# Kernel optimization log

Hardware: AMD Instinct MI355X
Metric: run time of the kernel (lower is better)

## Reference

```python
import jax, jax.numpy as jnp
import numpy as np
from jax.scipy.special import logsumexp

WORD_DIM = 512
SCRF_DIM = 256
N_TAGS = 12
ALLOWED_SPAN = 8
START_ID = 10
STOP_ID = 11
SEQ_LEN = 768
N_SPANS = 96


def _compute_scores(h, Wl, bl, Wr, br, Gl, bgl, Gr, bgr, Wt, bt, transitions):
    # h: [1, L, D] already projected by Dense
    Lc, D = h.shape[1], h.shape[2]
    scores = jnp.zeros((1, Lc, Lc, D), h.dtype)
    diag = jnp.arange(Lc)
    ht = h
    scores = scores.at[:, diag, diag].set(ht)
    for sl in range(1, min(ALLOWED_SPAN, Lc)):
        l, r = ht[:, :-1], ht[:, 1:]
        h_hat = 4.0 * jax.nn.sigmoid(l @ Wl.T + bl + r @ Wr.T + br) - 2.0
        # exp/normalize over 3 gates == softmax over gate axis
        g = (l @ Gl.T + bgl + r @ Gr.T + bgr).reshape(1, Lc - sl, 3, D)
        wgt = jax.nn.softmax(g, axis=2)
        ht = wgt[:, :, 0] * h_hat + wgt[:, :, 1] * l + wgt[:, :, 2] * r
        scores = scores.at[:, diag[:Lc - sl], diag[sl:]].set(ht)
    tagsc = scores @ Wt.T + bt  # [1, L, L, T]
    # final[b,i,j,prev,tag] = tagsc[b,i,j,tag] + transitions[prev,tag]
    return tagsc[:, :, :, None, :] + transitions[None, None, None]


def _forward_pass(s5):
    # s5: [1, L, L, T, T]; semi-Markov forward algorithm, windows of width <= ALLOWED_SPAN
    Lc, T = s5.shape[1], s5.shape[3]
    A = ALLOWED_SPAN
    i0 = jnp.arange(1, Lc + 1)
    k = jnp.arange(A)
    p = i0[:, None] - A + k[None, :]              # candidate span-start positions [L, A]
    m = p >= 0                                    # valid window mask (istarts = max(0, i-A))
    x = s5[0][jnp.clip(p, 0), (i0 - 1)[:, None]]  # [L, A, T, T] span scores ending at i-1
    buf0 = jnp.full((A, T), -10000.0, s5.dtype).at[A - 1, START_ID].set(0.0)

    def step(buf, inp):
        xi, mi = inp
        # tmp[k, prev, tag] = score + logalpha[start, prev]
        tmp = jnp.where(mi[:, None, None], xi + buf[:, :, None], -1e30)
        na = logsumexp(tmp, axis=(0, 1))  # [T]
        return jnp.concatenate([buf[1:], na[None]], axis=0), na

    _, alphas = jax.lax.scan(step, buf0, (x, m))
    return alphas[-1, :STOP_ID].sum()


def _gold_score(s5, tags):
    Lc, T = s5.shape[1], s5.shape[3]
    gf = tags[:, :, 0] * (Lc * T * T) + tags[:, :, 1] * (T * T) + tags[:, :, 2] * T + tags[:, :, 3]
    return jnp.take_along_axis(s5.reshape(1, -1), gf, axis=1).sum()


def setup_inputs() -> dict:
    key = jax.random.key(0)
    ks = jax.random.split(key, 16)
    D, W3 = SCRF_DIM, 3 * SCRF_DIM
    s = 0.05
    def w(k, shape):
        return jax.random.normal(k, shape, dtype=jnp.float32) * s
    return {
        "feats": jax.random.normal(ks[0], (1, SEQ_LEN, WORD_DIM), dtype=jnp.float32),
        "tags": jax.random.randint(ks[1], (1, N_SPANS, 4), 0, N_TAGS),
        "Wd": w(ks[2], (D, WORD_DIM)), "bd": jnp.zeros((D,), jnp.float32),
        "Wl": w(ks[3], (D, D)), "bl": jnp.zeros((D,), jnp.float32),
        "Wr": w(ks[4], (D, D)), "br": jnp.zeros((D,), jnp.float32),
        "Gl": w(ks[5], (W3, D)), "bgl": jnp.zeros((W3,), jnp.float32),
        "Gr": w(ks[6], (W3, D)), "bgr": jnp.zeros((W3,), jnp.float32),
        "Wt": w(ks[7], (N_TAGS, D)), "bt": jnp.zeros((N_TAGS,), jnp.float32),
        "transitions": w(ks[8], (N_TAGS, N_TAGS)),
    }


def reference(feats, tags, Wd, bd, Wl, bl, Wr, br, Gl, bgl, Gr, bgr, Wt, bt, transitions):
    h = feats @ Wd.T + bd  # Dense: word_dim -> scrf_dim
    s5 = _compute_scores(h, Wl, bl, Wr, br, Gl, bgl, Gr, bgr, Wt, bt, transitions)
    gold = _gold_score(s5, tags)
    logZ = _forward_pass(s5)
    return logZ - gold
```

## Files before the change

### kernel.cpp

```cpp
#include <hip/hip_runtime.h>

typedef __attribute__((ext_vector_type(8))) short short8;
typedef __attribute__((ext_vector_type(4))) float f32x4;

__device__ __forceinline__ float bf2f(short s) {
  return __uint_as_float(((unsigned)(unsigned short)s) << 16);
}
__device__ __forceinline__ unsigned short f2bf(float f) {
  unsigned u = __float_as_uint(f);
  unsigned rounding = 0x7fffu + ((u >> 16) & 1u);
  return (unsigned short)((u + rounding) >> 16);
}

__global__ void prep_kernel(const float* __restrict__ feats, const float* __restrict__ Wd,
                            const float* __restrict__ Wl, const float* __restrict__ Wr,
                            const float* __restrict__ Gl, const float* __restrict__ Gr,
                            const float* __restrict__ bl, const float* __restrict__ br,
                            const float* __restrict__ bgl, const float* __restrict__ bgr,
                            unsigned short* __restrict__ featsB, unsigned short* __restrict__ WdB,
                            unsigned short* __restrict__ WcB, float* __restrict__ bc)
{
  int idx = blockIdx.x * 256 + threadIdx.x;
  if (idx < 393216) {
    featsB[idx] = f2bf(feats[idx]);
  } else if (idx < 524288) {
    int j = idx - 393216;
    WdB[j] = f2bf(Wd[j]);
  } else if (idx < 1048576) {
    int j = idx - 524288;
    int o = j >> 9, k = j & 511;
    float v;
    if (k < 256) v = (o < 256) ? Wl[o*256 + k] : Gl[(o-256)*256 + k];
    else { int k2 = k - 256; v = (o < 256) ? Wr[o*256 + k2] : Gr[(o-256)*256 + k2]; }
    WcB[j] = f2bf(v);
  } else if (idx < 1049600) {
    int o = idx - 1048576;
    bc[o] = (o < 256) ? bl[o] + br[o] : bgl[o-256] + bgr[o-256];
  }
}

__global__ __launch_bounds__(256) void hgemm_kernel(const unsigned short* __restrict__ A,
                                                    const unsigned short* __restrict__ W,
                                                    const float* __restrict__ bd,
                                                    unsigned short* __restrict__ C)
{
  __shared__ __align__(16) unsigned short As[64][72];
  __shared__ __align__(16) unsigned short Ws[64][72];
  int p0 = blockIdx.x * 64;
  int n0 = blockIdx.y * 64;
  int tid = threadIdx.x;
  int wave = tid >> 6, lane = tid & 63;
  f32x4 acc[4];
  #pragma unroll
  for (int i = 0; i < 4; ++i)
    #pragma unroll
    for (int j = 0; j < 4; ++j) acc[i][j] = 0.f;

  int lr = tid >> 3;
  int c8 = (tid & 7) * 8;
  for (int kt = 0; kt < 8; ++kt) {
    int kb = kt * 64;
    #pragma unroll
    for (int rr = 0; rr < 64; rr += 32) {
      int row = lr + rr;
      *(short8*)(&As[row][c8]) = *(const short8*)(A + (size_t)(p0 + row)*512 + kb + c8);
      *(short8*)(&Ws[row][c8]) = *(const short8*)(W + (size_t)(n0 + row)*512 + kb + c8);
    }
    __syncthreads();
    int q8 = (lane >> 4) * 8;
    #pragma unroll
    for (int kk = 0; kk < 2; ++kk) {
      short8 b = *(const short8*)(&Ws[wave*16 + (lane & 15)][kk*32 + q8]);
      #pragma unroll
      for (int mt = 0; mt < 4; ++mt) {
        short8 a = *(const short8*)(&As[mt*16 + (lane & 15)][kk*32 + q8]);
        acc[mt] = __builtin_amdgcn_mfma_f32_16x16x32_bf16(a, b, acc[mt], 0, 0, 0);
      }
    }
    __syncthreads();
  }
  int o = n0 + wave*16 + (lane & 15);
  float bias = bd[o];
  #pragma unroll
  for (int mt = 0; mt < 4; ++mt)
    #pragma unroll
    for (int r = 0; r < 4; ++r) {
      int row = p0 + mt*16 + (lane >> 4)*4 + r;
      C[row*256 + o] = f2bf(acc[mt][r] + bias);
    }
}

__global__ __launch_bounds__(256) void iter_kernel(const unsigned short* __restrict__ htp,
                                                   const unsigned short* __restrict__ Wc,
                                                   const float* __restrict__ bc,
                                                   unsigned short* __restrict__ htn,
                                                   int Mvalid)
{
  __shared__ __align__(16) unsigned short As[64][72];
  __shared__ __align__(16) unsigned short Ws[64][72];
  __shared__ float Cs[64][64];
  int p0 = blockIdx.x * 64;
  int n0 = blockIdx.y * 16;
  int tid = threadIdx.x;
  int wave = tid >> 6, lane = tid & 63;
  f32x4 acc[4];
  #pragma unroll
  for (int i = 0; i < 4; ++i)
    #pragma unroll
    for (int j = 0; j < 4; ++j) acc[i][j] = 0.f;

  int lr = tid >> 3;
  int c8 = (tid & 7) * 8;
  for (int kt = 0; kt < 8; ++kt) {
    int kb = kt * 64;
    int shift = kb >> 8;
    int kcol = kb & 255;
    #pragma unroll
    for (int rr = 0; rr < 64; rr += 32) {
      int row = lr + rr;
      int grow = p0 + row + shift; if (grow > 767) grow = 767;
      *(short8*)(&As[row][c8]) = *(const short8*)(htp + (size_t)grow*256 + kcol + c8);
      int o = (row >> 4)*256 + n0 + (row & 15);
      *(short8*)(&Ws[row][c8]) = *(const short8*)(Wc + (size_t)o*512 + kb + c8);
    }
    __syncthreads();
    int q8 = (lane >> 4) * 8;
    #pragma unroll
    for (int kk = 0; kk < 2; ++kk) {
      short8 b = *(const short8*)(&Ws[wave*16 + (lane & 15)][kk*32 + q8]);
      #pragma unroll
      for (int mt = 0; mt < 4; ++mt) {
        short8 a = *(const short8*)(&As[mt*16 + (lane & 15)][kk*32 + q8]);
        acc[mt] = __builtin_amdgcn_mfma_f32_16x16x32_bf16(a, b, acc[mt], 0, 0, 0);
      }
    }
    __syncthreads();
  }
  #pragma unroll
  for (int mt = 0; mt < 4; ++mt)
    #pragma unroll
    for (int r = 0; r < 4; ++r)
      Cs[mt*16 + (lane >> 4)*4 + r][wave*16 + (lane & 15)] = acc[mt][r];
  __syncthreads();

  int dl = tid & 15;
  int d = n0 + dl;
  float bz = bc[d], b0 = bc[256 + d], b1 = bc[512 + d], b2v = bc[768 + d];
  for (int pr = tid >> 4; pr < 64; pr += 16) {
    int p = p0 + pr;
    if (p >= Mvalid) continue;
    float z  = Cs[pr][dl]      + bz;
    float g0 = Cs[pr][16 + dl] + b0;
    float g1 = Cs[pr][32 + dl] + b1;
    float g2 = Cs[pr][48 + dl] + b2v;
    float l = bf2f((short)htp[p*256 + d]);
    float r = bf2f((short)htp[(p+1)*256 + d]);
    float hh = 4.f / (1.f + __expf(-z)) - 2.f;
    float mg = fmaxf(g0, fmaxf(g1, g2));
    float e0 = __expf(g0 - mg), e1 = __expf(g1 - mg), e2 = __expf(g2 - mg);
    float inv = 1.f / (e0 + e1 + e2);
    htn[p*256 + d] = f2bf((e0*hh + e1*l + e2*r) * inv);
  }
}

__global__ __launch_bounds__(128) void band_kernel(const unsigned short* __restrict__ htall,
                                                   const float* __restrict__ Wt,
                                                   const float* __restrict__ bt,
                                                   float* __restrict__ Bband,
                                                   float* __restrict__ Xn,
                                                   float* __restrict__ mu)
{
  __shared__ __align__(16) unsigned short rows[8][264];
  __shared__ float sred[96];
  __shared__ float smu;
  int i = blockIdx.x + 1;
  int tid = threadIdx.x;
  for (int q = tid; q < 256; q += 128) {
    int k = q >> 5, cc = (q & 31) * 8;
    int p = i - 8 + k, sl = 7 - k;
    short8 v;
    if (p >= 0) {
      v = *(const short8*)(htall + ((size_t)sl*768 + p)*256 + cc);
    } else {
      for (int j = 0; j < 8; ++j) v[j] = 0;
    }
    *(short8*)(&rows[k][cc]) = v;
  }
  __syncthreads();
  float res = -1e30f;
  if (tid < 96) {
    int t = tid >> 3, k = tid & 7;
    int p = i - 8 + k;
    if (p >= 0) {
      float acc = 0.f;
      for (int dch = 0; dch < 256; dch += 8) {
        float4 wa = *(const float4*)(Wt + t*256 + dch);
        float4 wb = *(const float4*)(Wt + t*256 + dch + 4);
        short8 hv = *(const short8*)(&rows[k][dch]);
        acc += wa.x*bf2f(hv[0]) + wa.y*bf2f(hv[1]) + wa.z*bf2f(hv[2]) + wa.w*bf2f(hv[3])
             + wb.x*bf2f(hv[4]) + wb.y*bf2f(hv[5]) + wb.z*bf2f(hv[6]) + wb.w*bf2f(hv[7]);
      }
      res = acc + bt[t];
    }
    Bband[(size_t)i*96 + tid] = res;
    sred[tid] = res;
  }
  __syncthreads();
  if (tid < 32) {
    float m = fmaxf(sred[tid], fmaxf(sred[tid+32], sred[tid+64]));
    #pragma unroll
    for (int off = 16; off; off >>= 1) m = fmaxf(m, __shfl_down(m, off));
    if (tid == 0) { mu[i] = m; smu = m; }
  }
  __syncthreads();
  if (tid < 96) Xn[(size_t)i*96 + tid] = __expf(res - smu);
}

__global__ __launch_bounds__(256) void chunkT_kernel(const float* __restrict__ Xn,
                                                     const float* __restrict__ mu,
                                                     const float* __restrict__ trans,
                                                     float* __restrict__ T,
                                                     float* __restrict__ C0)
{
  int chunk = blockIdx.y;
  int a = chunk * 16;
  int tid = threadIdx.x;
  if (blockIdx.x == 0 && tid == 0) C0[chunk] = 0.f;
  int wv = tid >> 6;
  int lane = tid & 63;
  int g = lane / 12;
  int t = lane - g * 12;
  int cidx = blockIdx.x * 20 + wv * 5 + g;
  bool active = (g < 5) && (cidx < 96);
  int c = active ? cidx : 95;
  int s = c / 12, tau = c - s * 12;
  float Etc[12];
  #pragma unroll
  for (int j = 0; j < 12; ++j) Etc[j] = __expf(trans[j*12 + t]);
  float NA[8], V[8];
  #pragma unroll
  for (int j = 0; j < 8; ++j) { NA[j] = 0.f; V[j] = 0.f; }
  #pragma unroll
  for (int j = 0; j < 8; ++j) if (j == s) {
    NA[j] = (t == tau) ? 1.f : 0.f;
    V[j]  = Etc[tau];
  }
  int gb = (g * 12) * 4;
  #pragma unroll
  for (int m = 1; m <= 16; ++m) {
    const float* xr = Xn + (size_t)(a + m) * 96 + t * 8;
    float4 x0 = *(const float4*)xr;
    float4 x1 = *(const float4*)(xr + 4);
    float sf = __expf(-mu[a + m]);
    float na = x0.x*V[0] + x0.y*V[1] + x0.z*V[2] + x0.w*V[3]
             + x1.x*V[4] + x1.y*V[5] + x1.z*V[6] + x1.w*V[7];
    int nai = __float_as_int(na);
    float nb[12];
    #pragma unroll
    for (int j = 0; j < 12; ++j)
      nb[j] = __int_as_float(__builtin_amdgcn_ds_bpermute(gb + j*4, nai));
    float p0 = nb[0]*Etc[0] + nb[1]*Etc[1] + nb[2]*Etc[2]  + nb[3]*Etc[3];
    float p1 = nb[4]*Etc[4] + nb[5]*Etc[5] + nb[6]*Etc[6]  + nb[7]*Etc[7];
    float p2 = nb[8]*Etc[8] + nb[9]*Etc[9] + nb[10]*Etc[10] + nb[11]*Etc[11];
    float v = (p0 + p1) + p2;
    #pragma unroll
    for (int k = 0; k < 7; ++k) { NA[k] = NA[k+1]*sf; V[k] = V[k+1]*sf; }
    NA[7] = na; V[7] = v;
  }
  if (active) {
    float* dst = T + (size_t)chunk * 9216 + c;
    #pragma unroll
    for (int j = 0; j < 8; ++j) dst[(size_t)(j*12 + t) * 96] = NA[j];
  }
}

#define TPAD 100
__global__ __launch_bounds__(256) void treemul_kernel(const float* __restrict__ Tin,
                                                      const float* __restrict__ Cin,
                                                      float* __restrict__ Tout,
                                                      float* __restrict__ Cout)
{
  __shared__ float Bs[96 * TPAD];
  __shared__ float Acs[96 * TPAD];
  __shared__ float red[8];
  int j = blockIdx.y;
  int cs = blockIdx.x * 48;
  const float* Ag = Tin + (size_t)(2*j) * 9216;
  const float* Bg = Tin + (size_t)(2*j + 1) * 9216;
  int tid = threadIdx.x;
  int wv = tid >> 6, lane = tid & 63;

  float4 av[9], bv[9];
  const float* ap = Ag + tid * 36;
  const float* bp = Bg + tid * 36;
  #pragma unroll
  for (int q = 0; q < 9; ++q) av[q] = *(const float4*)(ap + q*4);
  #pragma unroll
  for (int q = 0; q < 9; ++q) bv[q] = *(const float4*)(bp + q*4);
  float ma = 0.f, mb = 0.f;
  #pragma unroll
  for (int q = 0; q < 9; ++q) {
    ma = fmaxf(ma, fmaxf(fmaxf(av[q].x, av[q].y), fmaxf(av[q].z, av[q].w)));
    mb = fmaxf(mb, fmaxf(fmaxf(bv[q].x, bv[q].y), fmaxf(bv[q].z, bv[q].w)));
  }
  #pragma unroll
  for (int off = 32; off; off >>= 1) {
    ma = fmaxf(ma, __shfl_down(ma, off));
    mb = fmaxf(mb, __shfl_down(mb, off));
  }
  if (lane == 0) { red[wv] = ma; red[4 + wv] = mb; }
  __syncthreads();
  float fa = fmaxf(fmaxf(red[0], red[1]), fmaxf(red[2], red[3]));
  float fb = fmaxf(fmaxf(red[4], red[5]), fmaxf(red[6], red[7]));
  float ia = 1.0f / fa, ib = 1.0f / fb;

  #pragma unroll
  for (int q = 0; q < 9; ++q) {
    int e = tid*36 + q*4;
    int r = e / 96, k = e - r*96;
    float4 b = bv[q];
    b.x *= ib; b.y *= ib; b.z *= ib; b.w *= ib;
    *(float4*)&Bs[r*TPAD + k] = b;
    float4 a = av[q];
    Acs[(k+0)*TPAD + r] = a.x * ia;
    Acs[(k+1)*TPAD + r] = a.y * ia;
    Acs[(k+2)*TPAD + r] = a.z * ia;
    Acs[(k+3)*TPAD + r] = a.w * ia;
  }
  __syncthreads();

  int tr = tid >> 4, tc = tid & 15;
  int r0 = tr * 6, c0 = cs + tc * 3;
  float acc[6][3];
  #pragma unroll
  for (int i = 0; i < 6; ++i)
    #pragma unroll
    for (int m = 0; m < 3; ++m) acc[i][m] = 0.f;
  for (int k = 0; k < 96; k += 4) {
    float4 a0 = *(const float4*)&Acs[(c0+0)*TPAD + k];
    float4 a1 = *(const float4*)&Acs[(c0+1)*TPAD + k];
    float4 a2 = *(const float4*)&Acs[(c0+2)*TPAD + k];
    #pragma unroll
    for (int i = 0; i < 6; ++i) {
      float4 b = *(const float4*)&Bs[(r0+i)*TPAD + k];
      acc[i][0] += b.x*a0.x + b.y*a0.y + b.z*a0.z + b.w*a0.w;
      acc[i][1] += b.x*a1.x + b.y*a1.y + b.z*a1.z + b.w*a1.w;
      acc[i][2] += b.x*a2.x + b.y*a2.y + b.z*a2.z + b.w*a2.w;
    }
  }
  float* op = Tout + (size_t)j * 9216;
  #pragma unroll
  for (int i = 0; i < 6; ++i)
    #pragma unroll
    for (int m = 0; m < 3; ++m)
      op[(size_t)(r0+i)*96 + c0 + m] = acc[i][m];
  if (blockIdx.x == 0 && tid == 0)
    Cout[j] = Cin[2*j] + Cin[2*j + 1] + __logf(fa) + __logf(fb);
}

__global__ __launch_bounds__(256, 1) void final_kernel(const float* __restrict__ Tm,
    const float* __restrict__ Cm, const float* __restrict__ Bband,
    const float* __restrict__ mu, const float* __restrict__ trans,
    const float* __restrict__ bt, const int* __restrict__ tags,
    float* __restrict__ out)
{
  __shared__ float Qs[2][96 * TPAD];
  __shared__ float vv[4][96];
  __shared__ float red[8];
  __shared__ float redm[4];
  int tid = threadIdx.x;
  int wv = tid >> 6, lane = tid & 63;

  float4 P[9];
  const float* p0 = Tm + tid * 36;
  #pragma unroll
  for (int q = 0; q < 9; ++q) P[q] = *(const float4*)(p0 + q*4);

  float gold = 0.f;
  if (tid < 96) {
    int a = tags[tid*4+0], b = tags[tid*4+1], cc = tags[tid*4+2], d = tags[tid*4+3];
    float v = trans[cc*12 + d];
    int sl = b - a;
    if (sl >= 0 && sl < 8) v += Bband[(size_t)(b+1)*96 + d*8 + (7 - sl)];
    else v += bt[d];
    gold = v;
  }
  float mp = 0.f;
  for (int q = tid; q < 768; q += 256) mp += mu[1 + q];
  #pragma unroll
  for (int off = 32; off; off >>= 1) {
    gold += __shfl_down(gold, off);
    mp   += __shfl_down(mp, off);
  }
  if (lane == 0) { red[wv] = gold; red[4 + wv] = mp; }

  #pragma unroll
  for (int q = 0; q < 9; ++q) {
    int e = tid*36 + q*4;
    int r = e / 96, k = e - r*96;
    *(float4*)&Qs[0][r*TPAD + k] = P[q];
  }
  if (tid < 96) vv[0][tid] = (tid == 94) ? 1.f : 0.f;
  __syncthreads();
  float gold_t = red[0] + red[1] + red[2] + red[3];
  float musum  = red[4] + red[5] + red[6] + red[7];
  float Ct = Cm[0] + Cm[1] + Cm[2];

  #pragma unroll
  for (int s = 0; s < 3; ++s) {
    if (s < 2) {
      const float* pn = Tm + (size_t)(s+1)*9216 + tid*36;
      #pragma unroll
      for (int q = 0; q < 9; ++q) P[q] = *(const float4*)(pn + q*4);
    }
    float acc = 0.f;
    if (tid < 96) {
      const float* Qr = &Qs[s & 1][tid * TPAD];
      #pragma unroll
      for (int k = 0; k < 96; k += 4) {
        float4 qv = *(const float4*)(Qr + k);
        float4 zv = *(const float4*)&vv[s][k];
        acc += qv.x*zv.x + qv.y*zv.y + qv.z*zv.z + qv.w*zv.w;
      }
    }
    float am = (tid < 96) ? acc : 0.f;
    #pragma unroll
    for (int off = 32; off; off >>= 1) am = fmaxf(am, __shfl_down(am, off));
    if (lane == 0) redm[wv] = am;
    __syncthreads();
    float mx = fmaxf(fmaxf(redm[0], redm[1]), fmaxf(redm[2], redm[3]));
    Ct += __logf(mx);
    if (tid < 96) vv[s+1][tid] = acc / mx;
    if (s < 2) {
      #pragma unroll
      for (int q = 0; q < 9; ++q) {
        int e = tid*36 + q*4;
        int r = e / 96, k = e - r*96;
        *(float4*)&Qs[(s+1)&1][r*TPAD + k] = P[q];
      }
    }
    __syncthreads();
  }
  if (tid == 0) {
    float lsum = 0.f;
    #pragma unroll
    for (int t = 0; t < 11; ++t) lsum += __logf(vv[3][84 + t]);
    out[0] = lsum + 11.f * (Ct + musum) - gold_t;
  }
}

extern "C" void kernel_launch(void* const* d_in, const int* in_sizes, int n_in,
                              void* d_out, int out_size, void* d_ws, size_t ws_size,
                              hipStream_t stream)
{
  const float* feats = (const float*)d_in[0];
  const int*   tags  = (const int*)  d_in[1];
  const float* Wd    = (const float*)d_in[2];
  const float* bd    = (const float*)d_in[3];
  const float* Wl    = (const float*)d_in[4];
  const float* bl    = (const float*)d_in[5];
  const float* Wr    = (const float*)d_in[6];
  const float* br    = (const float*)d_in[7];
  const float* Gl    = (const float*)d_in[8];
  const float* bgl   = (const float*)d_in[9];
  const float* Gr    = (const float*)d_in[10];
  const float* bgr   = (const float*)d_in[11];
  const float* Wt    = (const float*)d_in[12];
  const float* bt    = (const float*)d_in[13];
  const float* trans = (const float*)d_in[14];
  float* out = (float*)d_out;

  char* ws = (char*)d_ws;
  unsigned short* featsB = (unsigned short*)(ws + 0);
  unsigned short* WdB    = (unsigned short*)(ws + 786432);
  unsigned short* WcB    = (unsigned short*)(ws + 1048576);
  float*          bc     = (float*)         (ws + 2097152);
  unsigned short* ht     = (unsigned short*)(ws + 2101248);
  float*          Bband  = (float*)         (ws + 5246976);
  float*          Xn     = (float*)         (ws + 5542272);
  float*          muv    = (float*)         (ws + 5837568);
  float*          T      = (float*)         (ws + 5841664);
  float*          Tb     = (float*)         (ws + 0);
  float*          C0     = (float*)         (ws + 1048576);
  float*          Ca     = (float*)         (ws + 1048832);
  float*          Cb     = (float*)         (ws + 1049088);

  prep_kernel<<<4100, 256, 0, stream>>>(feats, Wd, Wl, Wr, Gl, Gr, bl, br, bgl, bgr,
                                        featsB, WdB, WcB, bc);
  hgemm_kernel<<<dim3(12, 4), 256, 0, stream>>>(featsB, WdB, bd, ht);
  for (int sl = 1; sl <= 7; ++sl)
    iter_kernel<<<dim3(12, 16), 256, 0, stream>>>(ht + (size_t)(sl-1)*768*256, WcB, bc,
                                                  ht + (size_t)sl*768*256, 768 - sl);
  band_kernel<<<768, 128, 0, stream>>>(ht, Wt, bt, Bband, Xn, muv);
  chunkT_kernel<<<dim3(5, 48), 256, 0, stream>>>(Xn, muv, trans, T, C0);
  treemul_kernel<<<dim3(2, 24), 256, 0, stream>>>(T,  C0, Tb, Ca);
  treemul_kernel<<<dim3(2, 12), 256, 0, stream>>>(Tb, Ca, T,  Cb);
  treemul_kernel<<<dim3(2,  6), 256, 0, stream>>>(T,  Cb, Tb, Ca);
  treemul_kernel<<<dim3(2,  3), 256, 0, stream>>>(Tb, Ca, T,  Cb);
  final_kernel<<<1, 256, 0, stream>>>(T, Cb, Bband, muv, trans, bt, tags, out);
}
```

Before: 207.2 us.

## Fuse post-prep kernels into one persistent kernel with software grid barriers

Replaces the chain of GEMM, seven iteration kernels, band, chunk, four tree-multiply and final kernels with a single persistent 256-block kernel. Stages are separated by atomic-counter grid barriers, with counters zeroed in the prep kernel. Shared memory is overlaid through a union. This removes about fifteen kernel launch gaps but depends on all blocks being co-resident, and it adds spin-wait barrier overhead.

```diff
diff --git a/kernel.cpp b/kernel.cpp
--- a/kernel.cpp
+++ b/kernel.cpp
@@ -2,6 +2,8 @@
 
 typedef __attribute__((ext_vector_type(8))) short short8;
 typedef __attribute__((ext_vector_type(4))) float f32x4;
+
+#define TPAD 100
 
 __device__ __forceinline__ float bf2f(short s) {
   return __uint_as_float(((unsigned)(unsigned short)s) << 16);
@@ -10,6 +12,24 @@
   unsigned u = __float_as_uint(f);
   unsigned rounding = 0x7fffu + ((u >> 16) & 1u);
   return (unsigned short)((u + rounding) >> 16);
+}
+
+union __align__(16) SmemU {
+  struct { unsigned short As[64][72]; unsigned short Ws[64][72]; float Cs[64][64]; } g;
+  struct { unsigned short rows[2][8][264]; float sred[2][96]; float smu[2]; } bn;
+  struct { float Bs[96 * TPAD]; float Acs[96 * TPAD]; float red[8]; } t;
+  struct { float Qs[2][96 * TPAD]; float vv[4][96]; float red[8]; float redm[4]; } f;
+};
+
+__device__ __forceinline__ void gridbar(unsigned* bar, unsigned nb) {
+  __syncthreads();
+  if (threadIdx.x == 0) {
+    __threadfence();
+    atomicAdd(bar, 1u);
+    while (atomicAdd(bar, 0u) < nb) __builtin_amdgcn_s_sleep(2);
+    __threadfence();
+  }
+  __syncthreads();
 }
 
 __global__ void prep_kernel(const float* __restrict__ feats, const float* __restrict__ Wd,
@@ -18,7 +38,8 @@
                             const float* __restrict__ bl, const float* __restrict__ br,
                             const float* __restrict__ bgl, const float* __restrict__ bgr,
                             unsigned short* __restrict__ featsB, unsigned short* __restrict__ WdB,
-                            unsigned short* __restrict__ WcB, float* __restrict__ bc)
+                            unsigned short* __restrict__ WcB, float* __restrict__ bc,
+                            unsigned* __restrict__ bars)
 {
   int idx = blockIdx.x * 256 + threadIdx.x;
   if (idx < 393216) {
@@ -36,259 +57,22 @@
   } else if (idx < 1049600) {
     int o = idx - 1048576;
     bc[o] = (o < 256) ? bl[o] + br[o] : bgl[o-256] + bgr[o-256];
-  }
-}
-
-__global__ __launch_bounds__(256) void hgemm_kernel(const unsigned short* __restrict__ A,
-                                                    const unsigned short* __restrict__ W,
-                                                    const float* __restrict__ bd,
-                                                    unsigned short* __restrict__ C)
+  } else {
+    int j = idx - 1049600;
+    if (j < 512) bars[j] = 0u;
+  }
+}
+
+__device__ __forceinline__ void treelevel(SmemU& sm,
+    const float* Tin, const float* Cin, float* Tout, float* Cout)
 {
-  __shared__ __align__(16) unsigned short As[64][72];
-  __shared__ __align__(16) unsigned short Ws[64][72];
-  int p0 = blockIdx.x * 64;
-  int n0 = blockIdx.y * 64;
-  int tid = threadIdx.x;
-  int wave = tid >> 6, lane = tid & 63;
-  f32x4 acc[4];
-  #pragma unroll
-  for (int i = 0; i < 4; ++i)
-    #pragma unroll
-    for (int j = 0; j < 4; ++j) acc[i][j] = 0.f;
-
-  int lr = tid >> 3;
-  int c8 = (tid & 7) * 8;
-  for (int kt = 0; kt < 8; ++kt) {
-    int kb = kt * 64;
-    #pragma unroll
-    for (int rr = 0; rr < 64; rr += 32) {
-      int row = lr + rr;
-      *(short8*)(&As[row][c8]) = *(const short8*)(A + (size_t)(p0 + row)*512 + kb + c8);
-      *(short8*)(&Ws[row][c8]) = *(const short8*)(W + (size_t)(n0 + row)*512 + kb + c8);
-    }
-    __syncthreads();
-    int q8 = (lane >> 4) * 8;
-    #pragma unroll
-    for (int kk = 0; kk < 2; ++kk) {
-      short8 b = *(const short8*)(&Ws[wave*16 + (lane & 15)][kk*32 + q8]);
-      #pragma unroll
-      for (int mt = 0; mt < 4; ++mt) {
-        short8 a = *(const short8*)(&As[mt*16 + (lane & 15)][kk*32 + q8]);
-        acc[mt] = __builtin_amdgcn_mfma_f32_16x16x32_bf16(a, b, acc[mt], 0, 0, 0);
-      }
-    }
-    __syncthreads();
-  }
-  int o = n0 + wave*16 + (lane & 15);
-  float bias = bd[o];
-  #pragma unroll
-  for (int mt = 0; mt < 4; ++mt)
-    #pragma unroll
-    for (int r = 0; r < 4; ++r) {
-      int row = p0 + mt*16 + (lane >> 4)*4 + r;
-      C[row*256 + o] = f2bf(acc[mt][r] + bias);
-    }
-}
-
-__global__ __launch_bounds__(256) void iter_kernel(const unsigned short* __restrict__ htp,
-                                                   const unsigned short* __restrict__ Wc,
-                                                   const float* __restrict__ bc,
-                                                   unsigned short* __restrict__ htn,
-                                                   int Mvalid)
-{
-  __shared__ __align__(16) unsigned short As[64][72];
-  __shared__ __align__(16) unsigned short Ws[64][72];
-  __shared__ float Cs[64][64];
-  int p0 = blockIdx.x * 64;
-  int n0 = blockIdx.y * 16;
-  int tid = threadIdx.x;
-  int wave = tid >> 6, lane = tid & 63;
-  f32x4 acc[4];
-  #pragma unroll
-  for (int i = 0; i < 4; ++i)
-    #pragma unroll
-    for (int j = 0; j < 4; ++j) acc[i][j] = 0.f;
-
-  int lr = tid >> 3;
-  int c8 = (tid & 7) * 8;
-  for (int kt = 0; kt < 8; ++kt) {
-    int kb = kt * 64;
-    int shift = kb >> 8;
-    int kcol = kb & 255;
-    #pragma unroll
-    for (int rr = 0; rr < 64; rr += 32) {
-      int row = lr + rr;
-      int grow = p0 + row + shift; if (grow > 767) grow = 767;
-      *(short8*)(&As[row][c8]) = *(const short8*)(htp + (size_t)grow*256 + kcol + c8);
-      int o = (row >> 4)*256 + n0 + (row & 15);
-      *(short8*)(&Ws[row][c8]) = *(const short8*)(Wc + (size_t)o*512 + kb + c8);
-    }
-    __syncthreads();
-    int q8 = (lane >> 4) * 8;
-    #pragma unroll
-    for (int kk = 0; kk < 2; ++kk) {
-      short8 b = *(const short8*)(&Ws[wave*16 + (lane & 15)][kk*32 + q8]);
-      #pragma unroll
-      for (int mt = 0; mt < 4; ++mt) {
-        short8 a = *(const short8*)(&As[mt*16 + (lane & 15)][kk*32 + q8]);
-        acc[mt] = __builtin_amdgcn_mfma_f32_16x16x32_bf16(a, b, acc[mt], 0, 0, 0);
-      }
-    }
-    __syncthreads();
-  }
-  #pragma unroll
-  for (int mt = 0; mt < 4; ++mt)
-    #pragma unroll
-    for (int r = 0; r < 4; ++r)
-      Cs[mt*16 + (lane >> 4)*4 + r][wave*16 + (lane & 15)] = acc[mt][r];
-  __syncthreads();
-
-  int dl = tid & 15;
-  int d = n0 + dl;
-  float bz = bc[d], b0 = bc[256 + d], b1 = bc[512 + d], b2v = bc[768 + d];
-  for (int pr = tid >> 4; pr < 64; pr += 16) {
-    int p = p0 + pr;
-    if (p >= Mvalid) continue;
-    float z  = Cs[pr][dl]      + bz;
-    float g0 = Cs[pr][16 + dl] + b0;
-    float g1 = Cs[pr][32 + dl] + b1;
-    float g2 = Cs[pr][48 + dl] + b2v;
-    float l = bf2f((short)htp[p*256 + d]);
-    float r = bf2f((short)htp[(p+1)*256 + d]);
-    float hh = 4.f / (1.f + __expf(-z)) - 2.f;
-    float mg = fmaxf(g0, fmaxf(g1, g2));
-    float e0 = __expf(g0 - mg), e1 = __expf(g1 - mg), e2 = __expf(g2 - mg);
-    float inv = 1.f / (e0 + e1 + e2);
-    htn[p*256 + d] = f2bf((e0*hh + e1*l + e2*r) * inv);
-  }
-}
-
-__global__ __launch_bounds__(128) void band_kernel(const unsigned short* __restrict__ htall,
-                                                   const float* __restrict__ Wt,
-                                                   const float* __restrict__ bt,
-                                                   float* __restrict__ Bband,
-                                                   float* __restrict__ Xn,
-                                                   float* __restrict__ mu)
-{
-  __shared__ __align__(16) unsigned short rows[8][264];
-  __shared__ float sred[96];
-  __shared__ float smu;
-  int i = blockIdx.x + 1;
-  int tid = threadIdx.x;
-  for (int q = tid; q < 256; q += 128) {
-    int k = q >> 5, cc = (q & 31) * 8;
-    int p = i - 8 + k, sl = 7 - k;
-    short8 v;
-    if (p >= 0) {
-      v = *(const short8*)(htall + ((size_t)sl*768 + p)*256 + cc);
-    } else {
-      for (int j = 0; j < 8; ++j) v[j] = 0;
-    }
-    *(short8*)(&rows[k][cc]) = v;
-  }
-  __syncthreads();
-  float res = -1e30f;
-  if (tid < 96) {
-    int t = tid >> 3, k = tid & 7;
-    int p = i - 8 + k;
-    if (p >= 0) {
-      float acc = 0.f;
-      for (int dch = 0; dch < 256; dch += 8) {
-        float4 wa = *(const float4*)(Wt + t*256 + dch);
-        float4 wb = *(const float4*)(Wt + t*256 + dch + 4);
-        short8 hv = *(const short8*)(&rows[k][dch]);
-        acc += wa.x*bf2f(hv[0]) + wa.y*bf2f(hv[1]) + wa.z*bf2f(hv[2]) + wa.w*bf2f(hv[3])
-             + wb.x*bf2f(hv[4]) + wb.y*bf2f(hv[5]) + wb.z*bf2f(hv[6]) + wb.w*bf2f(hv[7]);
-      }
-      res = acc + bt[t];
-    }
-    Bband[(size_t)i*96 + tid] = res;
-    sred[tid] = res;
-  }
-  __syncthreads();
-  if (tid < 32) {
-    float m = fmaxf(sred[tid], fmaxf(sred[tid+32], sred[tid+64]));
-    #pragma unroll
-    for (int off = 16; off; off >>= 1) m = fmaxf(m, __shfl_down(m, off));
-    if (tid == 0) { mu[i] = m; smu = m; }
-  }
-  __syncthreads();
-  if (tid < 96) Xn[(size_t)i*96 + tid] = __expf(res - smu);
-}
-
-__global__ __launch_bounds__(256) void chunkT_kernel(const float* __restrict__ Xn,
-                                                     const float* __restrict__ mu,
-                                                     const float* __restrict__ trans,
-                                                     float* __restrict__ T,
-                                                     float* __restrict__ C0)
-{
-  int chunk = blockIdx.y;
-  int a = chunk * 16;
-  int tid = threadIdx.x;
-  if (blockIdx.x == 0 && tid == 0) C0[chunk] = 0.f;
-  int wv = tid >> 6;
-  int lane = tid & 63;
-  int g = lane / 12;
-  int t = lane - g * 12;
-  int cidx = blockIdx.x * 20 + wv * 5 + g;
-  bool active = (g < 5) && (cidx < 96);
-  int c = active ? cidx : 95;
-  int s = c / 12, tau = c - s * 12;
-  float Etc[12];
-  #pragma unroll
-  for (int j = 0; j < 12; ++j) Etc[j] = __expf(trans[j*12 + t]);
-  float NA[8], V[8];
-  #pragma unroll
-  for (int j = 0; j < 8; ++j) { NA[j] = 0.f; V[j] = 0.f; }
-  #pragma unroll
-  for (int j = 0; j < 8; ++j) if (j == s) {
-    NA[j] = (t == tau) ? 1.f : 0.f;
-    V[j]  = Etc[tau];
-  }
-  int gb = (g * 12) * 4;
-  #pragma unroll
-  for (int m = 1; m <= 16; ++m) {
-    const float* xr = Xn + (size_t)(a + m) * 96 + t * 8;
-    float4 x0 = *(const float4*)xr;
-    float4 x1 = *(const float4*)(xr + 4);
-    float sf = __expf(-mu[a + m]);
-    float na = x0.x*V[0] + x0.y*V[1] + x0.z*V[2] + x0.w*V[3]
-             + x1.x*V[4] + x1.y*V[5] + x1.z*V[6] + x1.w*V[7];
-    int nai = __float_as_int(na);
-    float nb[12];
-    #pragma unroll
-    for (int j = 0; j < 12; ++j)
-      nb[j] = __int_as_float(__builtin_amdgcn_ds_bpermute(gb + j*4, nai));
-    float p0 = nb[0]*Etc[0] + nb[1]*Etc[1] + nb[2]*Etc[2]  + nb[3]*Etc[3];
-    float p1 = nb[4]*Etc[4] + nb[5]*Etc[5] + nb[6]*Etc[6]  + nb[7]*Etc[7];
-    float p2 = nb[8]*Etc[8] + nb[9]*Etc[9] + nb[10]*Etc[10] + nb[11]*Etc[11];
-    float v = (p0 + p1) + p2;
-    #pragma unroll
-    for (int k = 0; k < 7; ++k) { NA[k] = NA[k+1]*sf; V[k] = V[k+1]*sf; }
-    NA[7] = na; V[7] = v;
-  }
-  if (active) {
-    float* dst = T + (size_t)chunk * 9216 + c;
-    #pragma unroll
-    for (int j = 0; j < 8; ++j) dst[(size_t)(j*12 + t) * 96] = NA[j];
-  }
-}
-
-#define TPAD 100
-__global__ __launch_bounds__(256) void treemul_kernel(const float* __restrict__ Tin,
-                                                      const float* __restrict__ Cin,
-                                                      float* __restrict__ Tout,
-                                                      float* __restrict__ Cout)
-{
-  __shared__ float Bs[96 * TPAD];
-  __shared__ float Acs[96 * TPAD];
-  __shared__ float red[8];
-  int j = blockIdx.y;
-  int cs = blockIdx.x * 48;
+  const int bid = blockIdx.x;
+  const int tid = threadIdx.x;
+  const int wv = tid >> 6, lane = tid & 63;
+  const int j = bid >> 1;
+  const int cs = (bid & 1) * 48;
   const float* Ag = Tin + (size_t)(2*j) * 9216;
   const float* Bg = Tin + (size_t)(2*j + 1) * 9216;
-  int tid = threadIdx.x;
-  int wv = tid >> 6, lane = tid & 63;
 
   float4 av[9], bv[9];
   const float* ap = Ag + tid * 36;
@@ -308,24 +92,24 @@
     ma = fmaxf(ma, __shfl_down(ma, off));
     mb = fmaxf(mb, __shfl_down(mb, off));
   }
-  if (lane == 0) { red[wv] = ma; red[4 + wv] = mb; }
+  if (lane == 0) { sm.t.red[wv] = ma; sm.t.red[4 + wv] = mb; }
   __syncthreads();
-  float fa = fmaxf(fmaxf(red[0], red[1]), fmaxf(red[2], red[3]));
-  float fb = fmaxf(fmaxf(red[4], red[5]), fmaxf(red[6], red[7]));
+  float fa = fmaxf(fmaxf(sm.t.red[0], sm.t.red[1]), fmaxf(sm.t.red[2], sm.t.red[3]));
+  float fb = fmaxf(fmaxf(sm.t.red[4], sm.t.red[5]), fmaxf(sm.t.red[6], sm.t.red[7]));
   float ia = 1.0f / fa, ib = 1.0f / fb;
 
   #pragma unroll
   for (int q = 0; q < 9; ++q) {
     int e = tid*36 + q*4;
     int r = e / 96, k = e - r*96;
-    float4 b = bv[q];
-    b.x *= ib; b.y *= ib; b.z *= ib; b.w *= ib;
-    *(float4*)&Bs[r*TPAD + k] = b;
-    float4 a = av[q];
-    Acs[(k+0)*TPAD + r] = a.x * ia;
-    Acs[(k+1)*TPAD + r] = a.y * ia;
-    Acs[(k+2)*TPAD + r] = a.z * ia;
-    Acs[(k+3)*TPAD + r] = a.w * ia;
+    float4 bb = bv[q];
+    bb.x *= ib; bb.y *= ib; bb.z *= ib; bb.w *= ib;
+    *(float4*)&sm.t.Bs[r*TPAD + k] = bb;
+    float4 aa = av[q];
+    sm.t.Acs[(k+0)*TPAD + r] = aa.x * ia;
+    sm.t.Acs[(k+1)*TPAD + r] = aa.y * ia;
+    sm.t.Acs[(k+2)*TPAD + r] = aa.z * ia;
+    sm.t.Acs[(k+3)*TPAD + r] = aa.w * ia;
   }
   __syncthreads();
 
@@ -337,12 +121,12 @@
     #pragma unroll
     for (int m = 0; m < 3; ++m) acc[i][m] = 0.f;
   for (int k = 0; k < 96; k += 4) {
-    float4 a0 = *(const float4*)&Acs[(c0+0)*TPAD + k];
-    float4 a1 = *(const float4*)&Acs[(c0+1)*TPAD + k];
-    float4 a2 = *(const float4*)&Acs[(c0+2)*TPAD + k];
+    float4 a0 = *(const float4*)&sm.t.Acs[(c0+0)*TPAD + k];
+    float4 a1 = *(const float4*)&sm.t.Acs[(c0+1)*TPAD + k];
+    float4 a2 = *(const float4*)&sm.t.Acs[(c0+2)*TPAD + k];
     #pragma unroll
     for (int i = 0; i < 6; ++i) {
-      float4 b = *(const float4*)&Bs[(r0+i)*TPAD + k];
+      float4 b = *(const float4*)&sm.t.Bs[(r0+i)*TPAD + k];
       acc[i][0] += b.x*a0.x + b.y*a0.y + b.z*a0.z + b.w*a0.w;
       acc[i][1] += b.x*a1.x + b.y*a1.y + b.z*a1.z + b.w*a1.w;
       acc[i][2] += b.x*a2.x + b.y*a2.y + b.z*a2.z + b.w*a2.w;
@@ -354,98 +138,326 @@
     #pragma unroll
     for (int m = 0; m < 3; ++m)
       op[(size_t)(r0+i)*96 + c0 + m] = acc[i][m];
-  if (blockIdx.x == 0 && tid == 0)
+  if ((bid & 1) == 0 && tid == 0)
     Cout[j] = Cin[2*j] + Cin[2*j + 1] + __logf(fa) + __logf(fb);
 }
 
-__global__ __launch_bounds__(256, 1) void final_kernel(const float* __restrict__ Tm,
-    const float* __restrict__ Cm, const float* __restrict__ Bband,
-    const float* __restrict__ mu, const float* __restrict__ trans,
-    const float* __restrict__ bt, const int* __restrict__ tags,
-    float* __restrict__ out)
+__global__ __launch_bounds__(256, 2) void mega_kernel(
+    const unsigned short* featsB, const unsigned short* WdB,
+    const float* bd, const unsigned short* WcB, const float* bc,
+    unsigned short* ht, const float* Wt, const float* bt,
+    float* Bband, float* Xn, float* muv, const float* trans,
+    const int* tags, float* T, float* Tb, float* C0, float* Ca, float* Cb,
+    float* out, unsigned* bars)
 {
-  __shared__ float Qs[2][96 * TPAD];
-  __shared__ float vv[4][96];
-  __shared__ float red[8];
-  __shared__ float redm[4];
-  int tid = threadIdx.x;
-  int wv = tid >> 6, lane = tid & 63;
-
-  float4 P[9];
-  const float* p0 = Tm + tid * 36;
-  #pragma unroll
-  for (int q = 0; q < 9; ++q) P[q] = *(const float4*)(p0 + q*4);
-
-  float gold = 0.f;
-  if (tid < 96) {
-    int a = tags[tid*4+0], b = tags[tid*4+1], cc = tags[tid*4+2], d = tags[tid*4+3];
-    float v = trans[cc*12 + d];
-    int sl = b - a;
-    if (sl >= 0 && sl < 8) v += Bband[(size_t)(b+1)*96 + d*8 + (7 - sl)];
-    else v += bt[d];
-    gold = v;
-  }
-  float mp = 0.f;
-  for (int q = tid; q < 768; q += 256) mp += mu[1 + q];
-  #pragma unroll
-  for (int off = 32; off; off >>= 1) {
-    gold += __shfl_down(gold, off);
-    mp   += __shfl_down(mp, off);
-  }
-  if (lane == 0) { red[wv] = gold; red[4 + wv] = mp; }
-
-  #pragma unroll
-  for (int q = 0; q < 9; ++q) {
-    int e = tid*36 + q*4;
-    int r = e / 96, k = e - r*96;
-    *(float4*)&Qs[0][r*TPAD + k] = P[q];
-  }
-  if (tid < 96) vv[0][tid] = (tid == 94) ? 1.f : 0.f;
-  __syncthreads();
-  float gold_t = red[0] + red[1] + red[2] + red[3];
-  float musum  = red[4] + red[5] + red[6] + red[7];
-  float Ct = Cm[0] + Cm[1] + Cm[2];
-
-  #pragma unroll
-  for (int s = 0; s < 3; ++s) {
-    if (s < 2) {
-      const float* pn = Tm + (size_t)(s+1)*9216 + tid*36;
-      #pragma unroll
-      for (int q = 0; q < 9; ++q) P[q] = *(const float4*)(pn + q*4);
-    }
-    float acc = 0.f;
+  __shared__ SmemU sm;
+  const int bid = blockIdx.x;
+  const int tid = threadIdx.x;
+  const int wave = tid >> 6, lane = tid & 63;
+
+  if (bid < 48) {
+    const int p0 = (bid % 12) * 64;
+    const int n0 = (bid / 12) * 64;
+    f32x4 acc[4];
+    #pragma unroll
+    for (int i = 0; i < 4; ++i)
+      #pragma unroll
+      for (int j = 0; j < 4; ++j) acc[i][j] = 0.f;
+    const int lr = tid >> 3;
+    const int c8 = (tid & 7) * 8;
+    for (int kt = 0; kt < 8; ++kt) {
+      int kb = kt * 64;
+      #pragma unroll
+      for (int rr = 0; rr < 64; rr += 32) {
+        int row = lr + rr;
+        *(short8*)(&sm.g.As[row][c8]) = *(const short8*)(featsB + (size_t)(p0 + row)*512 + kb + c8);
+        *(short8*)(&sm.g.Ws[row][c8]) = *(const short8*)(WdB + (size_t)(n0 + row)*512 + kb + c8);
+      }
+      __syncthreads();
+      int q8 = (lane >> 4) * 8;
+      #pragma unroll
+      for (int kk = 0; kk < 2; ++kk) {
+        short8 bfr = *(const short8*)(&sm.g.Ws[wave*16 + (lane & 15)][kk*32 + q8]);
+        #pragma unroll
+        for (int mt = 0; mt < 4; ++mt) {
+          short8 afr = *(const short8*)(&sm.g.As[mt*16 + (lane & 15)][kk*32 + q8]);
+          acc[mt] = __builtin_amdgcn_mfma_f32_16x16x32_bf16(afr, bfr, acc[mt], 0, 0, 0);
+        }
+      }
+      __syncthreads();
+    }
+    int o = n0 + wave*16 + (lane & 15);
+    float bias = bd[o];
+    #pragma unroll
+    for (int mt = 0; mt < 4; ++mt)
+      #pragma unroll
+      for (int r = 0; r < 4; ++r) {
+        int row = p0 + mt*16 + (lane >> 4)*4 + r;
+        ht[row*256 + o] = f2bf(acc[mt][r] + bias);
+      }
+  }
+  gridbar(bars + 0*32, 256);
+
+  for (int sl = 1; sl <= 7; ++sl) {
+    if (bid < 192) {
+      const unsigned short* htp = ht + (size_t)(sl - 1) * 196608;
+      unsigned short* htn = ht + (size_t)sl * 196608;
+      const int Mvalid = 768 - sl;
+      const int p0 = (bid % 12) * 64;
+      const int n0 = (bid / 12) * 16;
+      f32x4 acc[4];
+      #pragma unroll
+      for (int i = 0; i < 4; ++i)
+        #pragma unroll
+        for (int j = 0; j < 4; ++j) acc[i][j] = 0.f;
+      const int lr = tid >> 3;
+      const int c8 = (tid & 7) * 8;
+      for (int kt = 0; kt < 8; ++kt) {
+        int kb = kt * 64;
+        int shift = kb >> 8;
+        int kcol = kb & 255;
+        #pragma unroll
+        for (int rr = 0; rr < 64; rr += 32) {
+          int row = lr + rr;
+          int grow = p0 + row + shift; if (grow > 767) grow = 767;
+          *(short8*)(&sm.g.As[row][c8]) = *(const short8*)(htp + (size_t)grow*256 + kcol + c8);
+          int o = (row >> 4)*256 + n0 + (row & 15);
+          *(short8*)(&sm.g.Ws[row][c8]) = *(const short8*)(WcB + (size_t)o*512 + kb + c8);
+        }
+        __syncthreads();
+        int q8 = (lane >> 4) * 8;
+        #pragma unroll
+        for (int kk = 0; kk < 2; ++kk) {
+          short8 bfr = *(const short8*)(&sm.g.Ws[wave*16 + (lane & 15)][kk*32 + q8]);
+          #pragma unroll
+          for (int mt = 0; mt < 4; ++mt) {
+            short8 afr = *(const short8*)(&sm.g.As[mt*16 + (lane & 15)][kk*32 + q8]);
+            acc[mt] = __builtin_amdgcn_mfma_f32_16x16x32_bf16(afr, bfr, acc[mt], 0, 0, 0);
+          }
+        }
+        __syncthreads();
+      }
+      #pragma unroll
+      for (int mt = 0; mt < 4; ++mt)
+        #pragma unroll
+        for (int r = 0; r < 4; ++r)
+          sm.g.Cs[mt*16 + (lane >> 4)*4 + r][wave*16 + (lane & 15)] = acc[mt][r];
+      __syncthreads();
+
+      int dl = tid & 15;
+      int d = n0 + dl;
+      float bz = bc[d], b0 = bc[256 + d], b1 = bc[512 + d], b2v = bc[768 + d];
+      for (int pr = tid >> 4; pr < 64; pr += 16) {
+        int p = p0 + pr;
+        if (p >= Mvalid) continue;
+        float z  = sm.g.Cs[pr][dl]      + bz;
+        float g0 = sm.g.Cs[pr][16 + dl] + b0;
+        float g1 = sm.g.Cs[pr][32 + dl] + b1;
+        float g2 = sm.g.Cs[pr][48 + dl] + b2v;
+        float l = bf2f((short)htp[p*256 + d]);
+        float r = bf2f((short)htp[(p+1)*256 + d]);
+        float hh = 4.f / (1.f + __expf(-z)) - 2.f;
+        float mg = fmaxf(g0, fmaxf(g1, g2));
+        float e0 = __expf(g0 - mg), e1 = __expf(g1 - mg), e2 = __expf(g2 - mg);
+        float inv = 1.f / (e0 + e1 + e2);
+        htn[p*256 + d] = f2bf((e0*hh + e1*l + e2*r) * inv);
+      }
+    }
+    gridbar(bars + sl*32, 256);
+  }
+
+  for (int task = bid; task < 384; task += 256) {
+    const int half = tid >> 7;
+    const int t2 = tid & 127;
+    const int i = 2*task + 1 + half;
+    for (int q = t2; q < 256; q += 128) {
+      int k = q >> 5, cc = (q & 31) * 8;
+      int p = i - 8 + k, slx = 7 - k;
+      short8 v;
+      if (p >= 0) {
+        v = *(const short8*)(ht + ((size_t)slx*768 + p)*256 + cc);
+      } else {
+        #pragma unroll
+        for (int j = 0; j < 8; ++j) v[j] = 0;
+      }
+      *(short8*)(&sm.bn.rows[half][k][cc]) = v;
+    }
+    __syncthreads();
+    float res = -1e30f;
+    if (t2 < 96) {
+      int t = t2 >> 3, k = t2 & 7;
+      int p = i - 8 + k;
+      if (p >= 0) {
+        float acc = 0.f;
+        for (int dch = 0; dch < 256; dch += 8) {
+          float4 wa = *(const float4*)(Wt + t*256 + dch);
+          float4 wb = *(const float4*)(Wt + t*256 + dch + 4);
+          short8 hv = *(const short8*)(&sm.bn.rows[half][k][dch]);
+          acc += wa.x*bf2f(hv[0]) + wa.y*bf2f(hv[1]) + wa.z*bf2f(hv[2]) + wa.w*bf2f(hv[3])
+               + wb.x*bf2f(hv[4]) + wb.y*bf2f(hv[5]) + wb.z*bf2f(hv[6]) + wb.w*bf2f(hv[7]);
+        }
+        res = acc + bt[t];
+      }
+      Bband[(size_t)i*96 + t2] = res;
+      sm.bn.sred[half][t2] = res;
+    }
+    __syncthreads();
+    if (t2 < 32) {
+      float m = fmaxf(sm.bn.sred[half][t2],
+                 fmaxf(sm.bn.sred[half][t2+32], sm.bn.sred[half][t2+64]));
+      #pragma unroll
+      for (int off = 16; off; off >>= 1) m = fmaxf(m, __shfl_down(m, off));
+      if (t2 == 0) { muv[i] = m; sm.bn.smu[half] = m; }
+    }
+    __syncthreads();
+    if (t2 < 96) Xn[(size_t)i*96 + t2] = __expf(res - sm.bn.smu[half]);
+    __syncthreads();
+  }
+  gridbar(bars + 8*32, 256);
+
+  if (bid < 240) {
+    const int chunk = bid / 5;
+    const int bxx = bid % 5;
+    if (bxx == 0 && tid == 0) C0[chunk] = 0.f;
+    const int a = chunk * 16;
+    const int g = lane / 12;
+    const int t = lane - g * 12;
+    const int cidx = bxx * 20 + wave * 5 + g;
+    const bool active = (g < 5) && (cidx < 96);
+    const int c = active ? cidx : 95;
+    const int s = c / 12, tau = c - s * 12;
+    float Etc[12];
+    #pragma unroll
+    for (int jj = 0; jj < 12; ++jj) Etc[jj] = __expf(trans[jj*12 + t]);
+    float NA[8], V[8];
+    #pragma unroll
+    for (int jj = 0; jj < 8; ++jj) { NA[jj] = 0.f; V[jj] = 0.f; }
+    #pragma unroll
+    for (int jj = 0; jj < 8; ++jj) if (jj == s) {
+      NA[jj] = (t == tau) ? 1.f : 0.f;
+      V[jj]  = Etc[tau];
+    }
+    const int gbb = (g * 12) * 4;
+    #pragma unroll
+    for (int m = 1; m <= 16; ++m) {
+      const float* xr = Xn + (size_t)(a + m) * 96 + t * 8;
+      float4 x0 = *(const float4*)xr;
+      float4 x1 = *(const float4*)(xr + 4);
+      float sf = __expf(-muv[a + m]);
+      float na = x0.x*V[0] + x0.y*V[1] + x0.z*V[2] + x0.w*V[3]
+               + x1.x*V[4] + x1.y*V[5] + x1.z*V[6] + x1.w*V[7];
+      int nai = __float_as_int(na);
+      float nb[12];
+      #pragma unroll
+      for (int jj = 0; jj < 12; ++jj)
+        nb[jj] = __int_as_float(__builtin_amdgcn_ds_bpermute(gbb + jj*4, nai));
+      float pp0 = nb[0]*Etc[0] + nb[1]*Etc[1] + nb[2]*Etc[2]   + nb[3]*Etc[3];
+      float pp1 = nb[4]*Etc[4] + nb[5]*Etc[5] + nb[6]*Etc[6]   + nb[7]*Etc[7];
+      float pp2 = nb[8]*Etc[8] + nb[9]*Etc[9] + nb[10]*Etc[10] + nb[11]*Etc[11];
+      float v = (pp0 + pp1) + pp2;
+      #pragma unroll
+      for (int kq = 0; kq < 7; ++kq) { NA[kq] = NA[kq+1]*sf; V[kq] = V[kq+1]*sf; }
+      NA[7] = na; V[7] = v;
+    }
+    if (active) {
+      float* dst = T + (size_t)chunk * 9216 + c;
+      #pragma unroll
+      for (int jj = 0; jj < 8; ++jj) dst[(size_t)(jj*12 + t) * 96] = NA[jj];
+    }
+  }
+  gridbar(bars + 9*32, 256);
+
+  if (bid >= 48) return;
+  treelevel(sm, T, C0, Tb, Ca);
+  gridbar(bars + 10*32, 48);
+  if (bid >= 24) return;
+  treelevel(sm, Tb, Ca, T, Cb);
+  gridbar(bars + 11*32, 24);
+  if (bid >= 12) return;
+  treelevel(sm, T, Cb, Tb, Ca);
+  gridbar(bars + 12*32, 12);
+  if (bid >= 6) return;
+  treelevel(sm, Tb, Ca, T, Cb);
+  gridbar(bars + 13*32, 6);
+  if (bid) return;
+
+  {
+    float4 P[9];
+    const float* p0p = T + tid * 36;
+    #pragma unroll
+    for (int q = 0; q < 9; ++q) P[q] = *(const float4*)(p0p + q*4);
+
+    float gold = 0.f;
     if (tid < 96) {
-      const float* Qr = &Qs[s & 1][tid * TPAD];
-      #pragma unroll
-      for (int k = 0; k < 96; k += 4) {
-        float4 qv = *(const float4*)(Qr + k);
-        float4 zv = *(const float4*)&vv[s][k];
-        acc += qv.x*zv.x + qv.y*zv.y + qv.z*zv.z + qv.w*zv.w;
-      }
-    }
-    float am = (tid < 96) ? acc : 0.f;
-    #pragma unroll
-    for (int off = 32; off; off >>= 1) am = fmaxf(am, __shfl_down(am, off));
-    if (lane == 0) redm[wv] = am;
+      int a = tags[tid*4+0], b = tags[tid*4+1], cc = tags[tid*4+2], d = tags[tid*4+3];
+      float v = trans[cc*12 + d];
+      int sl = b - a;
+      if (sl >= 0 && sl < 8) v += Bband[(size_t)(b+1)*96 + d*8 + (7 - sl)];
+      else v += bt[d];
+      gold = v;
+    }
+    float mp = 0.f;
+    for (int q = tid; q < 768; q += 256) mp += muv[1 + q];
+    #pragma unroll
+    for (int off = 32; off; off >>= 1) {
+      gold += __shfl_down(gold, off);
+      mp   += __shfl_down(mp, off);
+    }
+    if (lane == 0) { sm.f.red[wave] = gold; sm.f.red[4 + wave] = mp; }
+
+    #pragma unroll
+    for (int q = 0; q < 9; ++q) {
+      int e = tid*36 + q*4;
+      int r = e / 96, k = e - r*96;
+      *(float4*)&sm.f.Qs[0][r*TPAD + k] = P[q];
+    }
+    if (tid < 96) sm.f.vv[0][tid] = (tid == 94) ? 1.f : 0.f;
     __syncthreads();
-    float mx = fmaxf(fmaxf(redm[0], redm[1]), fmaxf(redm[2], redm[3]));
-    Ct += __logf(mx);
-    if (tid < 96) vv[s+1][tid] = acc / mx;
-    if (s < 2) {
-      #pragma unroll
-      for (int q = 0; q < 9; ++q) {
-        int e = tid*36 + q*4;
-        int r = e / 96, k = e - r*96;
-        *(float4*)&Qs[(s+1)&1][r*TPAD + k] = P[q];
-      }
-    }
-    __syncthreads();
-  }
-  if (tid == 0) {
-    float lsum = 0.f;
-    #pragma unroll
-    for (int t = 0; t < 11; ++t) lsum += __logf(vv[3][84 + t]);
-    out[0] = lsum + 11.f * (Ct + musum) - gold_t;
+    float gold_t = sm.f.red[0] + sm.f.red[1] + sm.f.red[2] + sm.f.red[3];
+    float musum  = sm.f.red[4] + sm.f.red[5] + sm.f.red[6] + sm.f.red[7];
+    float Ct = Cb[0] + Cb[1] + Cb[2];
+
+    #pragma unroll
+    for (int s = 0; s < 3; ++s) {
+      if (s < 2) {
+        const float* pn = T + (size_t)(s+1)*9216 + tid*36;
+        #pragma unroll
+        for (int q = 0; q < 9; ++q) P[q] = *(const float4*)(pn + q*4);
+      }
+      float acc = 0.f;
+      if (tid < 96) {
+        const float* Qr = &sm.f.Qs[s & 1][tid * TPAD];
+        #pragma unroll
+        for (int k = 0; k < 96; k += 4) {
+          float4 qv = *(const float4*)(Qr + k);
+          float4 zv = *(const float4*)&sm.f.vv[s][k];
+          acc += qv.x*zv.x + qv.y*zv.y + qv.z*zv.z + qv.w*zv.w;
+        }
+      }
+      float am = (tid < 96) ? acc : 0.f;
+      #pragma unroll
+      for (int off = 32; off; off >>= 1) am = fmaxf(am, __shfl_down(am, off));
+      if (lane == 0) sm.f.redm[wave] = am;
+      __syncthreads();
+      float mx = fmaxf(fmaxf(sm.f.redm[0], sm.f.redm[1]), fmaxf(sm.f.redm[2], sm.f.redm[3]));
+      Ct += __logf(mx);
+      if (tid < 96) sm.f.vv[s+1][tid] = acc / mx;
+      if (s < 2) {
+        #pragma unroll
+        for (int q = 0; q < 9; ++q) {
+          int e = tid*36 + q*4;
+          int r = e / 96, k = e - r*96;
+          *(float4*)&sm.f.Qs[(s+1)&1][r*TPAD + k] = P[q];
+        }
+      }
+      __syncthreads();
+    }
+    if (tid == 0) {
+      float lsum = 0.f;
+      #pragma unroll
+      for (int t = 0; t < 11; ++t) lsum += __logf(sm.f.vv[3][84 + t]);
+      out[0] = lsum + 11.f * (Ct + musum) - gold_t;
+    }
   }
 }
 
@@ -484,18 +496,11 @@
   float*          C0     = (float*)         (ws + 1048576);
   float*          Ca     = (float*)         (ws + 1048832);
   float*          Cb     = (float*)         (ws + 1049088);
-
-  prep_kernel<<<4100, 256, 0, stream>>>(feats, Wd, Wl, Wr, Gl, Gr, bl, br, bgl, bgr,
-                                        featsB, WdB, WcB, bc);
-  hgemm_kernel<<<dim3(12, 4), 256, 0, stream>>>(featsB, WdB, bd, ht);
-  for (int sl = 1; sl <= 7; ++sl)
-    iter_kernel<<<dim3(12, 16), 256, 0, stream>>>(ht + (size_t)(sl-1)*768*256, WcB, bc,
-                                                  ht + (size_t)sl*768*256, 768 - sl);
-  band_kernel<<<768, 128, 0, stream>>>(ht, Wt, bt, Bband, Xn, muv);
-  chunkT_kernel<<<dim3(5, 48), 256, 0, stream>>>(Xn, muv, trans, T, C0);
-  treemul_kernel<<<dim3(2, 24), 256, 0, stream>>>(T,  C0, Tb, Ca);
-  treemul_kernel<<<dim3(2, 12), 256, 0, stream>>>(Tb, Ca, T,  Cb);
-  treemul_kernel<<<dim3(2,  6), 256, 0, stream>>>(T,  Cb, Tb, Ca);
-  treemul_kernel<<<dim3(2,  3), 256, 0, stream>>>(Tb, Ca, T,  Cb);
-  final_kernel<<<1, 256, 0, stream>>>(T, Cb, Bband, muv, trans, bt, tags, out);
-}
+  unsigned*       bars   = (unsigned*)      (ws + 7611136);
+
+  prep_kernel<<<4102, 256, 0, stream>>>(feats, Wd, Wl, Wr, Gl, Gr, bl, br, bgl, bgr,
+                                        featsB, WdB, WcB, bc, bars);
+  mega_kernel<<<256, 256, 0, stream>>>(featsB, WdB, bd, WcB, bc, ht, Wt, bt,
+                                       Bband, Xn, muv, trans, tags, T, Tb, C0, Ca, Cb,
+                                       out, bars);
+}
```

Result: slower. 391.7 us (+89.0%).
